# Kernel optimization log

Measured on AMD Instinct MI355X. Metric: run time of the kernel, lower is better.

## Reference

```python
import jax, jax.numpy as jnp
import numpy as np

N_NODES = 100000
N_EDGES = 1200000
D_FEAT = 64


def setup_inputs() -> dict:
    key = jax.random.key(0)
    k1, k2, k3, k4 = jax.random.split(key, 4)
    # row-sorted COO == CSR ordering (original sorts edge_index by source row)
    row = jnp.sort(jax.random.randint(k1, (N_EDGES,), 0, N_NODES, dtype=jnp.int32))
    col = jax.random.randint(k2, (N_EDGES,), 0, N_NODES, dtype=jnp.int32)
    vals = jax.random.uniform(k3, (N_EDGES,), dtype=jnp.float32)
    x = jax.random.normal(k4, (N_NODES, D_FEAT), dtype=jnp.float32)
    return {"x": x, "vals": vals, "row": row, "col": col}


def reference(x, vals, row, col):
    n = x.shape[0]
    # SpMM: out[r] = sum_{e: row[e]==r} vals[e] * x[col[e]]
    msgs = vals[:, None] * x[col]                      # [E, D]
    out = jax.ops.segment_sum(msgs, row, num_segments=n)  # [N, D]
    # degree = per-row nnz (crow_indices diff in the original), clamped to >=1
    deg = jax.ops.segment_sum(jnp.ones_like(vals), row, num_segments=n)
    deg = jnp.maximum(deg, 1.0)
    return out / deg[:, None]
```

## Files before the change

### kernel.cpp

```cpp
#include <hip/hip_runtime.h>

#define D_FEAT 64

__global__ void fill_ptr_kernel(const int* __restrict__ row,
                                int* __restrict__ ptr,
                                int n_rows, int n_edges) {
    int e = blockIdx.x * blockDim.x + threadIdx.x;
    if (e >= n_edges) return;
    int r = row[e];
    int rprev = (e == 0) ? -1 : row[e - 1];
    for (int q = rprev + 1; q <= r; ++q) ptr[q] = e;
    if (e == n_edges - 1) {
        for (int q = r + 1; q <= n_rows; ++q) ptr[q] = n_edges;
    }
}

__global__ __launch_bounds__(256) void spmm_kernel(
        const float* __restrict__ x,
        const float* __restrict__ vals,
        const int* __restrict__ col,
        const int* __restrict__ ptr,
        float* __restrict__ out,
        int n_rows) {
    int wave = (blockIdx.x * blockDim.x + threadIdx.x) >> 6;
    int lane = threadIdx.x & 63;
    if (wave >= n_rows) return;

    int sub = lane >> 4;
    int fl  = lane & 15;

    int start = ptr[wave];
    int end   = ptr[wave + 1];
    int deg   = end - start;

    float4 acc0 = make_float4(0.f, 0.f, 0.f, 0.f);
    float4 acc1 = make_float4(0.f, 0.f, 0.f, 0.f);

    for (int e = start + sub; e < end; e += 8) {
        int eb_raw = e + 4;
        int eb = eb_raw < end ? eb_raw : end - 1;

        int   ca = col[e];
        int   cb = col[eb];
        float va = vals[e];
        float vb = eb_raw < end ? vals[eb] : 0.0f;

        const float4 xa = *(const float4*)(x + (size_t)ca * D_FEAT + fl * 4);
        const float4 xb = *(const float4*)(x + (size_t)cb * D_FEAT + fl * 4);

        acc0.x = fmaf(va, xa.x, acc0.x);
        acc0.y = fmaf(va, xa.y, acc0.y);
        acc0.z = fmaf(va, xa.z, acc0.z);
        acc0.w = fmaf(va, xa.w, acc0.w);
        acc1.x = fmaf(vb, xb.x, acc1.x);
        acc1.y = fmaf(vb, xb.y, acc1.y);
        acc1.z = fmaf(vb, xb.z, acc1.z);
        acc1.w = fmaf(vb, xb.w, acc1.w);
    }

    float ax = acc0.x + acc1.x;
    float ay = acc0.y + acc1.y;
    float az = acc0.z + acc1.z;
    float aw = acc0.w + acc1.w;

    ax += __shfl_xor(ax, 16, 64); ay += __shfl_xor(ay, 16, 64);
    az += __shfl_xor(az, 16, 64); aw += __shfl_xor(aw, 16, 64);
    ax += __shfl_xor(ax, 32, 64); ay += __shfl_xor(ay, 32, 64);
    az += __shfl_xor(az, 32, 64); aw += __shfl_xor(aw, 32, 64);

    float inv = 1.0f / (float)(deg > 0 ? deg : 1);
    if (sub == 0) {
        float4 r = make_float4(ax * inv, ay * inv, az * inv, aw * inv);
        *(float4*)(out + (size_t)wave * D_FEAT + fl * 4) = r;
    }
}

extern "C" void kernel_launch(void* const* d_in, const int* in_sizes, int n_in,
                              void* d_out, int out_size, void* d_ws, size_t ws_size,
                              hipStream_t stream) {
    const float* x    = (const float*)d_in[0];
    const float* vals = (const float*)d_in[1];
    const int*   row  = (const int*)d_in[2];
    const int*   col  = (const int*)d_in[3];
    float* out = (float*)d_out;

    int n_edges = in_sizes[1];
    int n_rows  = out_size / D_FEAT;

    int* row_ptr = (int*)d_ws;

    {
        int threads = 256;
        int blocks = (n_edges + threads - 1) / threads;
        fill_ptr_kernel<<<blocks, threads, 0, stream>>>(row, row_ptr, n_rows, n_edges);
    }
    {
        int threads = 256;
        long total_threads = (long)n_rows * 64;
        int blocks = (int)((total_threads + threads - 1) / threads);
        spmm_kernel<<<blocks, threads, 0, stream>>>(x, vals, col, row_ptr, out, n_rows);
    }
}
```

Before: 126.4 us.

## Gather features from an fp16 copy of x to halve gather bandwidth

Adds a kernel that converts x to fp16 in workspace each call, then runs a new SpMM kernel that gathers half8 rows (8 lanes per edge, 8 edges per wave step) and accumulates in fp32. The goal is to halve the bytes moved by the random row gathers, which dominate this memory-bound SpMM. In exchange it adds a full conversion pass over x (read 25.6MB, write 12.8MB) and an extra launch, and fp16 rounding loses precision. The old fp32 path is kept as a fallback when the workspace is too small.

Result: no change. 124.3 us (-1.7%).

```diff
diff --git a/kernel.cpp b/kernel.cpp
--- a/kernel.cpp
+++ b/kernel.cpp
@@ -1,6 +1,20 @@
 #include <hip/hip_runtime.h>
 
 #define D_FEAT 64
+
+typedef _Float16 half4 __attribute__((ext_vector_type(4)));
+typedef _Float16 half8 __attribute__((ext_vector_type(8)));
+
+__global__ void convert_kernel(const float* __restrict__ x,
+                               _Float16* __restrict__ x16, int n_elems) {
+    int i = (blockIdx.x * blockDim.x + threadIdx.x) * 4;
+    if (i >= n_elems) return;
+    float4 v = *(const float4*)(x + i);
+    half4 h;
+    h.x = (_Float16)v.x; h.y = (_Float16)v.y;
+    h.z = (_Float16)v.z; h.w = (_Float16)v.w;
+    *(half4*)(x16 + i) = h;
+}
 
 __global__ void fill_ptr_kernel(const int* __restrict__ row,
                                 int* __restrict__ ptr,
@@ -15,6 +29,65 @@
     }
 }
 
+__global__ __launch_bounds__(256) void spmm16_kernel(
+        const _Float16* __restrict__ x16,
+        const float* __restrict__ vals,
+        const int* __restrict__ col,
+        const int* __restrict__ ptr,
+        float* __restrict__ out,
+        int n_rows) {
+    int wave = (blockIdx.x * blockDim.x + threadIdx.x) >> 6;
+    int lane = threadIdx.x & 63;
+    if (wave >= n_rows) return;
+
+    int sub = lane >> 3;
+    int fl  = lane & 7;
+
+    int start = ptr[wave];
+    int end   = ptr[wave + 1];
+    int deg   = end - start;
+
+    float a0[8] = {0,0,0,0,0,0,0,0};
+    float a1[8] = {0,0,0,0,0,0,0,0};
+
+    for (int e = start + sub; e < end; e += 16) {
+        int e1r = e + 8;
+        int e1  = e1r < end ? e1r : end - 1;
+
+        int   c0 = col[e];
+        int   c1 = col[e1];
+        float v0 = vals[e];
+        float v1 = e1r < end ? vals[e1] : 0.0f;
+
+        half8 h0 = *(const half8*)(x16 + (size_t)c0 * D_FEAT + fl * 8);
+        half8 h1 = *(const half8*)(x16 + (size_t)c1 * D_FEAT + fl * 8);
+
+        #pragma unroll
+        for (int k = 0; k < 8; ++k) {
+            a0[k] = fmaf(v0, (float)h0[k], a0[k]);
+            a1[k] = fmaf(v1, (float)h1[k], a1[k]);
+        }
+    }
+
+    #pragma unroll
+    for (int k = 0; k < 8; ++k) {
+        float t = a0[k] + a1[k];
+        t += __shfl_xor(t, 8, 64);
+        t += __shfl_xor(t, 16, 64);
+        t += __shfl_xor(t, 32, 64);
+        a0[k] = t;
+    }
+
+    float inv = 1.0f / (float)(deg > 0 ? deg : 1);
+    if (sub == 0) {
+        float* dst = out + (size_t)wave * D_FEAT + fl * 8;
+        float4 r0 = make_float4(a0[0]*inv, a0[1]*inv, a0[2]*inv, a0[3]*inv);
+        float4 r1 = make_float4(a0[4]*inv, a0[5]*inv, a0[6]*inv, a0[7]*inv);
+        *(float4*)dst = r0;
+        *(float4*)(dst + 4) = r1;
+    }
+}
+
 __global__ __launch_bounds__(256) void spmm_kernel(
         const float* __restrict__ x,
         const float* __restrict__ vals,
@@ -25,52 +98,36 @@
     int wave = (blockIdx.x * blockDim.x + threadIdx.x) >> 6;
     int lane = threadIdx.x & 63;
     if (wave >= n_rows) return;
-
     int sub = lane >> 4;
     int fl  = lane & 15;
-
     int start = ptr[wave];
     int end   = ptr[wave + 1];
     int deg   = end - start;
-
-    float4 acc0 = make_float4(0.f, 0.f, 0.f, 0.f);
-    float4 acc1 = make_float4(0.f, 0.f, 0.f, 0.f);
-
+    float4 acc0 = make_float4(0.f,0.f,0.f,0.f);
+    float4 acc1 = make_float4(0.f,0.f,0.f,0.f);
     for (int e = start + sub; e < end; e += 8) {
         int eb_raw = e + 4;
         int eb = eb_raw < end ? eb_raw : end - 1;
-
         int   ca = col[e];
         int   cb = col[eb];
         float va = vals[e];
         float vb = eb_raw < end ? vals[eb] : 0.0f;
-
         const float4 xa = *(const float4*)(x + (size_t)ca * D_FEAT + fl * 4);
         const float4 xb = *(const float4*)(x + (size_t)cb * D_FEAT + fl * 4);
-
-        acc0.x = fmaf(va, xa.x, acc0.x);
-        acc0.y = fmaf(va, xa.y, acc0.y);
-        acc0.z = fmaf(va, xa.z, acc0.z);
-        acc0.w = fmaf(va, xa.w, acc0.w);
-        acc1.x = fmaf(vb, xb.x, acc1.x);
-        acc1.y = fmaf(vb, xb.y, acc1.y);
-        acc1.z = fmaf(vb, xb.z, acc1.z);
-        acc1.w = fmaf(vb, xb.w, acc1.w);
+        acc0.x = fmaf(va, xa.x, acc0.x); acc0.y = fmaf(va, xa.y, acc0.y);
+        acc0.z = fmaf(va, xa.z, acc0.z); acc0.w = fmaf(va, xa.w, acc0.w);
+        acc1.x = fmaf(vb, xb.x, acc1.x); acc1.y = fmaf(vb, xb.y, acc1.y);
+        acc1.z = fmaf(vb, xb.z, acc1.z); acc1.w = fmaf(vb, xb.w, acc1.w);
     }
-
-    float ax = acc0.x + acc1.x;
-    float ay = acc0.y + acc1.y;
-    float az = acc0.z + acc1.z;
-    float aw = acc0.w + acc1.w;
-
+    float ax = acc0.x + acc1.x, ay = acc0.y + acc1.y;
+    float az = acc0.z + acc1.z, aw = acc0.w + acc1.w;
     ax += __shfl_xor(ax, 16, 64); ay += __shfl_xor(ay, 16, 64);
     az += __shfl_xor(az, 16, 64); aw += __shfl_xor(aw, 16, 64);
     ax += __shfl_xor(ax, 32, 64); ay += __shfl_xor(ay, 32, 64);
     az += __shfl_xor(az, 32, 64); aw += __shfl_xor(aw, 32, 64);
-
     float inv = 1.0f / (float)(deg > 0 ? deg : 1);
     if (sub == 0) {
-        float4 r = make_float4(ax * inv, ay * inv, az * inv, aw * inv);
+        float4 r = make_float4(ax*inv, ay*inv, az*inv, aw*inv);
         *(float4*)(out + (size_t)wave * D_FEAT + fl * 4) = r;
     }
 }
@@ -86,18 +143,30 @@
 
     int n_edges = in_sizes[1];
     int n_rows  = out_size / D_FEAT;
+    int n_x     = in_sizes[0];
 
     int* row_ptr = (int*)d_ws;
+    size_t ptr_bytes  = (size_t)(n_rows + 1) * sizeof(int);
+    size_t x16_off    = (ptr_bytes + 255) & ~(size_t)255;
+    size_t need       = x16_off + (size_t)n_x * sizeof(_Float16);
 
     {
         int threads = 256;
         int blocks = (n_edges + threads - 1) / threads;
         fill_ptr_kernel<<<blocks, threads, 0, stream>>>(row, row_ptr, n_rows, n_edges);
     }
-    {
-        int threads = 256;
-        long total_threads = (long)n_rows * 64;
-        int blocks = (int)((total_threads + threads - 1) / threads);
+
+    int threads = 256;
+    long total_threads = (long)n_rows * 64;
+    int blocks = (int)((total_threads + threads - 1) / threads);
+
+    if (ws_size >= need) {
+        _Float16* x16 = (_Float16*)((char*)d_ws + x16_off);
+        int cthreads = 256;
+        int cblocks = (n_x / 4 + cthreads - 1) / cthreads;
+        convert_kernel<<<cblocks, cthreads, 0, stream>>>(x, x16, n_x);
+        spmm16_kernel<<<blocks, threads, 0, stream>>>(x16, vals, col, row_ptr, out, n_rows);
+    } else {
         spmm_kernel<<<blocks, threads, 0, stream>>>(x, vals, col, row_ptr, out, n_rows);
     }
 }
```
